# Performance work log

Hardware: AMD Instinct MI355X
Metric: run time of the kernel (lower is better)

Reference implementation:

```python
import jax, jax.numpy as jnp
import numpy as np

B, T, N = 64, 500, 2048
THRESHOLD = 1.0
BETA_RES = 0.9      # beta_reservoir
BETA_IN = 0.8       # input_lif_beta
SPECTRAL_RADIUS = 0.9
INIT_A, INIT_B = -1.0, 1.0


def setup_inputs() -> dict:
    key = jax.random.key(0)
    k1, k2, k3 = jax.random.split(key, 3)
    x = jax.random.normal(k1, (B, T, 1), dtype=jnp.float32)
    w_in = jax.random.normal(k2, (1, 1), dtype=jnp.float32)      # input_fc weight (out=1, in=1)
    w_res_in = jax.random.normal(k3, (N, 1), dtype=jnp.float32)  # reservoir_fc weight (out=N, in=1)
    # Recurrent weights: uniform[a,b] then rescale to desired spectral radius (done in numpy, matches init-time torch code)
    rng = np.random.default_rng(0)
    W = rng.uniform(INIT_A, INIT_B, size=(N, N)).astype(np.float32)
    radius = np.abs(np.linalg.eigvals(W)).max()
    W = W * (SPECTRAL_RADIUS / radius)
    W_rec = jnp.asarray(W, dtype=jnp.float32)
    return {"x": x, "w_in": w_in, "w_res_in": w_res_in, "W_rec": W_rec}


def reference(x, w_in, w_res_in, W_rec):
    """Vmem input path: input LIF integrates without spiking; reservoir is an
    all-to-all recurrent LIF with zero reset. Returns (avg_firing_rate, spike_record, mem_record)."""
    dtype = x.dtype
    imem0 = jnp.zeros((x.shape[0], 1), dtype)
    mem0 = jnp.zeros((x.shape[0], N), dtype)
    spk0 = jnp.zeros((x.shape[0], N), dtype)

    def step(carry, x_t):
        imem, mem, spk = carry
        # input LIF membrane (no spike/reset in 'Vmem' mode)
        imem = BETA_IN * imem + x_t @ w_in.T                      # (B,1)
        cur = imem @ w_res_in.T                                   # (B,N)
        # reservoir RLeaky, zero reset based on previous spikes, recurrent all-to-all
        mem = BETA_RES * mem * (1.0 - spk) + cur + spk @ W_rec.T  # (B,N)
        spk = (mem > THRESHOLD).astype(dtype)
        return (imem, mem, spk), (spk, mem)

    xs = jnp.transpose(x, (1, 0, 2))  # (T,B,1)
    _, (spike_record, mem_record) = jax.lax.scan(step, (imem0, mem0, spk0), xs)
    avg_firing_rate = spike_record.mean()
    return avg_firing_rate, spike_record, mem_record
```

## Files before the change

### kernel.cpp

```cpp
#include <hip/hip_runtime.h>

typedef int v4i __attribute__((ext_vector_type(4)));

#define WMAX_OFF   0
#define CNT_OFF    4
#define EP_OFF     8
#define IMEM_OFF   64
#define PK_OFF     131072
#define FLAGS_OFF  196608
#define WFRAG_OFF  262144

__global__ void sr_prep(const float* __restrict__ x, const float* __restrict__ w_in,
                        float* __restrict__ imem, unsigned* wmax_bits, unsigned* cnt,
                        unsigned* ep) {
  int b = threadIdx.x;
  if (b == 64) *wmax_bits = 0u;
  if (b == 65) *cnt = 0u;
  if (b == 66) *ep += 1024u;
  if (b < 64) {
    float wi = w_in[0];
    float im = 0.0f;
    for (int t = 0; t < 500; ++t) {
      im = 0.8f * im + x[b * 500 + t] * wi;
      imem[t * 64 + b] = im;
    }
  }
}

__global__ void sr_wmax(const float* __restrict__ W, unsigned* wmax_bits) {
  __shared__ unsigned sm;
  if (threadIdx.x == 0) sm = 0u;
  __syncthreads();
  float m = 0.0f;
  for (size_t i = (size_t)blockIdx.x * 256 + threadIdx.x; i < 4194304ull; i += 262144ull)
    m = fmaxf(m, fabsf(W[i]));
  atomicMax(&sm, __float_as_uint(m));
  __syncthreads();
  if (threadIdx.x == 0) atomicMax(wmax_bits, sm);
}

__global__ void sr_wquant(const float* __restrict__ W, const unsigned* __restrict__ wmax_bits,
                          v4i* __restrict__ wfr) {
  __shared__ float ws[16][257];
  const int p = blockIdx.x >> 3;
  const int w = blockIdx.x & 7;
  const int tid = threadIdx.x;
  {
    int r = tid >> 5;
    int c0 = (tid & 31) * 8;
    const float* src = W + (size_t)(p * 16 + r) * 2048 + 256 * w + c0;
    #pragma unroll
    for (int j = 0; j < 8; ++j) ws[r][c0 + j] = src[j];
  }
  __syncthreads();
  const int fl = tid >> 6;
  const int kl = fl >> 1, sp = fl & 1;
  const int lane = tid & 63;
  const int col = lane & 15;
  const int q = lane >> 4;
  const float S = 32000.0f / __uint_as_float(*wmax_bits);
  int dw[4] = {0, 0, 0, 0};
  #pragma unroll
  for (int j = 0; j < 16; ++j) {
    int d = j >> 2, i = j & 3;
    float wv = ws[col][(4 * kl + q) * 16 + 4 * i + d];
    int qv = (int)rintf(wv * S);
    int hi = (qv + 128) >> 8;
    int lo = qv - (hi << 8);
    int v = sp ? lo : hi;
    dw[d] |= (v & 255) << (8 * i);
  }
  v4i o; o[0] = dw[0]; o[1] = dw[1]; o[2] = dw[2]; o[3] = dw[3];
  wfr[(size_t)((((p * 8 + w) * 4 + kl) * 2 + sp)) * 64 + lane] = o;
}

__global__ __launch_bounds__(512, 2)
void sr_main(const float* __restrict__ imem, const v4i* __restrict__ wfr,
             unsigned* pk, unsigned* flags, const unsigned* __restrict__ ep,
             const float* __restrict__ w_res, const unsigned* __restrict__ wmax_bits,
             unsigned* cnt_g, float* __restrict__ out) {
  extern __shared__ char smem_raw[];
  unsigned* spk_lds = (unsigned*)smem_raw;
  v4i* redv = (v4i*)(smem_raw + 16384);
  int* outl = (int*)(smem_raw + 49152);

  const int p = blockIdx.x;
  const int tid = threadIdx.x;
  const int w = tid >> 6;
  const int lane = tid & 63;
  const int q = lane >> 4;
  const int col = lane & 15;
  const unsigned base = *ep;

  v4i wf[4][2];
  #pragma unroll
  for (int kl = 0; kl < 4; ++kl)
    #pragma unroll
    for (int sp = 0; sp < 2; ++sp)
      wf[kl][sp] = wfr[(size_t)((((p * 8 + w) * 4 + kl) * 2 + sp)) * 64 + lane];

  const int be = tid >> 3;
  const int h = tid & 7;
  const int nl = h * 2;
  const float wr0 = w_res[p * 16 + nl + 0];
  const float wr1 = w_res[p * 16 + nl + 1];
  float mem0 = 0, mem1 = 0, sp0 = 0, sp1 = 0;
  int cnt = 0;
  const float invS = __uint_as_float(*wmax_bits) / 32000.0f;
  const v4i vzero = {0, 0, 0, 0};
  const int pubshift = (h >> 1) * 8 + 2 * (h & 1) + 4 * (be & 1);
  const int sh2 = (col & 1) * 4;
  const int cc = col >> 1;

  for (int t = 0; t < 500; ++t) {
    float im = imem[t * 64 + be];
    float rec0 = 0, rec1 = 0;
    if (t > 0) {
      const unsigned target = base + (unsigned)t;
      if (tid < 128) {
        unsigned* fp = flags + (size_t)(t & 1) * 128 + tid;
        int guard = 0;
        while (__hip_atomic_load(fp, __ATOMIC_RELAXED, __HIP_MEMORY_SCOPE_AGENT) != target) {
          __builtin_amdgcn_s_sleep(1);
          if (++guard > (1 << 20)) break;
        }
      }
      __syncthreads();

      {
        const unsigned* src = pk + (size_t)(t & 1) * 4096 + tid;
        unsigned qw[8];
        #pragma unroll
        for (int j = 0; j < 8; ++j)
          qw[j] = __hip_atomic_load(src + 512 * j, __ATOMIC_RELAXED, __HIP_MEMORY_SCOPE_AGENT);
        #pragma unroll
        for (int j = 0; j < 8; ++j) {
          int P = tid + 512 * j;
          int idx = (P & ~31) | ((P & 31) ^ (((P >> 5) & 3) << 3));
          spk_lds[idx] = qw[j];
        }
      }
      __syncthreads();

      unsigned ww[16];
      #pragma unroll
      for (int f = 0; f < 16; ++f) {
        int kl = f & 3, bt = f >> 2;
        ww[f] = spk_lds[(16 * w + 4 * kl + q) * 32 + ((bt * 8 + cc) ^ (q << 3))];
      }

      v4i acc[4][2];
      #pragma unroll
      for (int bt = 0; bt < 4; ++bt) { acc[bt][0] = vzero; acc[bt][1] = vzero; }
      #pragma unroll
      for (int f = 0; f < 16; ++f) {
        int kl = f & 3, bt = f >> 2;
        unsigned wbs = ww[f] >> sh2;
        v4i a;
        a[0] = (int)((wbs >> 0) & 0x01010101u);
        a[1] = (int)((wbs >> 1) & 0x01010101u);
        a[2] = (int)((wbs >> 2) & 0x01010101u);
        a[3] = (int)((wbs >> 3) & 0x01010101u);
        acc[bt][0] = __builtin_amdgcn_mfma_i32_16x16x64_i8(a, wf[kl][0], acc[bt][0], 0, 0, 0);
        acc[bt][1] = __builtin_amdgcn_mfma_i32_16x16x64_i8(a, wf[kl][1], acc[bt][1], 0, 0, 0);
      }
      #pragma unroll
      for (int bt = 0; bt < 4; ++bt) {
        v4i c = acc[bt][0] * 256 + acc[bt][1];
        redv[(w * 4 + bt) * 64 + lane] = c;
      }
      __syncthreads();
      if (w < 4) {
        v4i s = vzero;
        #pragma unroll
        for (int ww2 = 0; ww2 < 8; ++ww2) s += redv[(ww2 * 4 + w) * 64 + lane];
        int ob = (w * 16 + (lane >> 4) * 4) * 16 + (lane & 15);
        outl[ob]      = s[0];
        outl[ob + 16] = s[1];
        outl[ob + 32] = s[2];
        outl[ob + 48] = s[3];
      }
      __syncthreads();
      int2 rv = *(const int2*)(outl + be * 16 + nl);
      rec0 = (float)rv.x * invS;
      rec1 = (float)rv.y * invS;
    }

    mem0 = 0.9f * mem0 * (1.0f - sp0) + im * wr0 + rec0;
    mem1 = 0.9f * mem1 * (1.0f - sp1) + im * wr1 + rec1;
    int s0i = mem0 > 1.0f, s1i = mem1 > 1.0f;
    sp0 = (float)s0i; sp1 = (float)s1i;

    unsigned v = ((unsigned)(s0i | (s1i << 1))) << pubshift;
    v |= (unsigned)__shfl_xor((int)v, 1);
    v |= (unsigned)__shfl_xor((int)v, 2);
    v |= (unsigned)__shfl_xor((int)v, 4);
    v |= (unsigned)__shfl_xor((int)v, 8);
    if ((tid & 15) == 0)
      __hip_atomic_store(&pk[(size_t)((t + 1) & 1) * 4096 + p * 32 + (tid >> 4)], v,
                         __ATOMIC_RELAXED, __HIP_MEMORY_SCOPE_AGENT);
    __syncthreads();
    if (tid == 0)
      __hip_atomic_store(&flags[(size_t)((t + 1) & 1) * 128 + p], base + (unsigned)(t + 1),
                         __ATOMIC_RELAXED, __HIP_MEMORY_SCOPE_AGENT);
    cnt += s0i + s1i;

    size_t sb = 1ull + (size_t)t * 131072ull + (size_t)be * 2048ull + (size_t)(p * 16 + nl);
    __builtin_nontemporal_store(sp0, out + sb + 0);
    __builtin_nontemporal_store(sp1, out + sb + 1);
    __builtin_nontemporal_store(mem0, out + sb + 65536000ull + 0);
    __builtin_nontemporal_store(mem1, out + sb + 65536000ull + 1);
  }

  __syncthreads();
  int* csh = (int*)smem_raw;
  if (tid == 0) csh[0] = 0;
  __syncthreads();
  atomicAdd(csh, cnt);
  __syncthreads();
  if (tid == 0) atomicAdd(cnt_g, (unsigned)csh[0]);
}

__global__ void sr_fin(const unsigned* __restrict__ cnt, float* __restrict__ out) {
  out[0] = (float)((double)(*cnt) / 65536000.0);
}

extern "C" void kernel_launch(void* const* d_in, const int* in_sizes, int n_in,
                              void* d_out, int out_size, void* d_ws, size_t ws_size,
                              hipStream_t stream) {
  const float* x     = (const float*)d_in[0];
  const float* w_in  = (const float*)d_in[1];
  const float* w_res = (const float*)d_in[2];
  const float* W     = (const float*)d_in[3];
  float* out = (float*)d_out;
  char* ws = (char*)d_ws;

  unsigned* wmax_bits = (unsigned*)(ws + WMAX_OFF);
  unsigned* cntp      = (unsigned*)(ws + CNT_OFF);
  unsigned* ep        = (unsigned*)(ws + EP_OFF);
  float* imem         = (float*)(ws + IMEM_OFF);
  unsigned* pkt       = (unsigned*)(ws + PK_OFF);
  unsigned* flg       = (unsigned*)(ws + FLAGS_OFF);
  v4i* wfr            = (v4i*)(ws + WFRAG_OFF);

  sr_prep<<<1, 128, 0, stream>>>(x, w_in, imem, wmax_bits, cntp, ep);
  sr_wmax<<<1024, 256, 0, stream>>>(W, wmax_bits);
  sr_wquant<<<1024, 512, 0, stream>>>(W, wmax_bits, wfr);
  sr_main<<<128, 512, 53248, stream>>>(imem, wfr, pkt, flg, ep, w_res, wmax_bits, cntp, out);
  sr_fin<<<1, 1, 0, stream>>>(cntp, out);
}
```

Baseline: 2.113 ms.

## Embed epoch tags in 64-bit spike packets to drop flag barrier and LDS staging

Each spike word is now published as a 64-bit value whose upper half holds the step epoch. Consumers poll their own 16 packets directly from global memory until every tag matches. This removes the per-block flag array, the producer-side barrier before the flag store, the flag spin by 128 threads, and the LDS staging of spike words along with two block barriers. In exchange every thread polls 16 global words per step, adding L2 traffic and retries. The prep kernel also batches its x loads in chunks of 10.

```diff
diff --git a/kernel.cpp b/kernel.cpp
--- a/kernel.cpp
+++ b/kernel.cpp
@@ -7,7 +7,6 @@
 #define EP_OFF     8
 #define IMEM_OFF   64
 #define PK_OFF     131072
-#define FLAGS_OFF  196608
 #define WFRAG_OFF  262144
 
 __global__ void sr_prep(const float* __restrict__ x, const float* __restrict__ w_in,
@@ -20,9 +19,15 @@
   if (b < 64) {
     float wi = w_in[0];
     float im = 0.0f;
-    for (int t = 0; t < 500; ++t) {
-      im = 0.8f * im + x[b * 500 + t] * wi;
-      imem[t * 64 + b] = im;
+    for (int t0 = 0; t0 < 500; t0 += 10) {
+      float xs[10];
+      #pragma unroll
+      for (int j = 0; j < 10; ++j) xs[j] = x[b * 500 + t0 + j];
+      #pragma unroll
+      for (int j = 0; j < 10; ++j) {
+        im = 0.8f * im + xs[j] * wi;
+        imem[(t0 + j) * 64 + b] = im;
+      }
     }
   }
 }
@@ -76,13 +81,12 @@
 
 __global__ __launch_bounds__(512, 2)
 void sr_main(const float* __restrict__ imem, const v4i* __restrict__ wfr,
-             unsigned* pk, unsigned* flags, const unsigned* __restrict__ ep,
+             unsigned long long* pk, const unsigned* __restrict__ ep,
              const float* __restrict__ w_res, const unsigned* __restrict__ wmax_bits,
              unsigned* cnt_g, float* __restrict__ out) {
   extern __shared__ char smem_raw[];
-  unsigned* spk_lds = (unsigned*)smem_raw;
-  v4i* redv = (v4i*)(smem_raw + 16384);
-  int* outl = (int*)(smem_raw + 49152);
+  v4i* redv = (v4i*)smem_raw;
+  int* outl = (int*)(smem_raw + 32768);
 
   const int p = blockIdx.x;
   const int tid = threadIdx.x;
@@ -112,50 +116,40 @@
   const int sh2 = (col & 1) * 4;
   const int cc = col >> 1;
 
+  int pidx[16];
+  #pragma unroll
+  for (int f = 0; f < 16; ++f) {
+    int kl = f & 3, bt = f >> 2;
+    pidx[f] = (16 * w + 4 * kl + q) * 32 + bt * 8 + cc;
+  }
+
   for (int t = 0; t < 500; ++t) {
     float im = imem[t * 64 + be];
     float rec0 = 0, rec1 = 0;
     if (t > 0) {
-      const unsigned target = base + (unsigned)t;
-      if (tid < 128) {
-        unsigned* fp = flags + (size_t)(t & 1) * 128 + tid;
-        int guard = 0;
-        while (__hip_atomic_load(fp, __ATOMIC_RELAXED, __HIP_MEMORY_SCOPE_AGENT) != target) {
-          __builtin_amdgcn_s_sleep(1);
-          if (++guard > (1 << 20)) break;
-        }
-      }
-      __syncthreads();
-
-      {
-        const unsigned* src = pk + (size_t)(t & 1) * 4096 + tid;
-        unsigned qw[8];
+      const unsigned tgt = base + (unsigned)t;
+      const unsigned long long* src = pk + (size_t)((t - 1) & 1) * 4096;
+      unsigned long long qp[16];
+      bool ok = false;
+      int guard = 0;
+      do {
         #pragma unroll
-        for (int j = 0; j < 8; ++j)
-          qw[j] = __hip_atomic_load(src + 512 * j, __ATOMIC_RELAXED, __HIP_MEMORY_SCOPE_AGENT);
+        for (int f = 0; f < 16; ++f)
+          qp[f] = __hip_atomic_load(src + pidx[f], __ATOMIC_RELAXED, __HIP_MEMORY_SCOPE_AGENT);
+        unsigned bad = 0;
         #pragma unroll
-        for (int j = 0; j < 8; ++j) {
-          int P = tid + 512 * j;
-          int idx = (P & ~31) | ((P & 31) ^ (((P >> 5) & 3) << 3));
-          spk_lds[idx] = qw[j];
-        }
-      }
-      __syncthreads();
-
-      unsigned ww[16];
+        for (int f = 0; f < 16; ++f) bad |= (unsigned)(qp[f] >> 32) ^ tgt;
+        ok = (bad == 0);
+        if (!ok) __builtin_amdgcn_s_sleep(1);
+      } while (!ok && ++guard < (1 << 20));
+
+      v4i acc[4][2];
+      #pragma unroll
+      for (int bt = 0; bt < 4; ++bt) { acc[bt][0] = vzero; acc[bt][1] = vzero; }
       #pragma unroll
       for (int f = 0; f < 16; ++f) {
         int kl = f & 3, bt = f >> 2;
-        ww[f] = spk_lds[(16 * w + 4 * kl + q) * 32 + ((bt * 8 + cc) ^ (q << 3))];
-      }
-
-      v4i acc[4][2];
-      #pragma unroll
-      for (int bt = 0; bt < 4; ++bt) { acc[bt][0] = vzero; acc[bt][1] = vzero; }
-      #pragma unroll
-      for (int f = 0; f < 16; ++f) {
-        int kl = f & 3, bt = f >> 2;
-        unsigned wbs = ww[f] >> sh2;
+        unsigned wbs = (unsigned)qp[f] >> sh2;
         v4i a;
         a[0] = (int)((wbs >> 0) & 0x01010101u);
         a[1] = (int)((wbs >> 1) & 0x01010101u);
@@ -196,13 +190,12 @@
     v |= (unsigned)__shfl_xor((int)v, 2);
     v |= (unsigned)__shfl_xor((int)v, 4);
     v |= (unsigned)__shfl_xor((int)v, 8);
-    if ((tid & 15) == 0)
-      __hip_atomic_store(&pk[(size_t)((t + 1) & 1) * 4096 + p * 32 + (tid >> 4)], v,
+    if ((tid & 15) == 0) {
+      unsigned long long pkt =
+          (unsigned long long)v | ((unsigned long long)(base + (unsigned)(t + 1)) << 32);
+      __hip_atomic_store(&pk[(size_t)(t & 1) * 4096 + p * 32 + (tid >> 4)], pkt,
                          __ATOMIC_RELAXED, __HIP_MEMORY_SCOPE_AGENT);
-    __syncthreads();
-    if (tid == 0)
-      __hip_atomic_store(&flags[(size_t)((t + 1) & 1) * 128 + p], base + (unsigned)(t + 1),
-                         __ATOMIC_RELAXED, __HIP_MEMORY_SCOPE_AGENT);
+    }
     cnt += s0i + s1i;
 
     size_t sb = 1ull + (size_t)t * 131072ull + (size_t)be * 2048ull + (size_t)(p * 16 + nl);
@@ -239,13 +232,12 @@
   unsigned* cntp      = (unsigned*)(ws + CNT_OFF);
   unsigned* ep        = (unsigned*)(ws + EP_OFF);
   float* imem         = (float*)(ws + IMEM_OFF);
-  unsigned* pkt       = (unsigned*)(ws + PK_OFF);
-  unsigned* flg       = (unsigned*)(ws + FLAGS_OFF);
+  unsigned long long* pkt = (unsigned long long*)(ws + PK_OFF);
   v4i* wfr            = (v4i*)(ws + WFRAG_OFF);
 
   sr_prep<<<1, 128, 0, stream>>>(x, w_in, imem, wmax_bits, cntp, ep);
   sr_wmax<<<1024, 256, 0, stream>>>(W, wmax_bits);
   sr_wquant<<<1024, 512, 0, stream>>>(W, wmax_bits, wfr);
-  sr_main<<<128, 512, 53248, stream>>>(imem, wfr, pkt, flg, ep, w_res, wmax_bits, cntp, out);
+  sr_main<<<128, 512, 36864, stream>>>(imem, wfr, pkt, ep, w_res, wmax_bits, cntp, out);
   sr_fin<<<1, 1, 0, stream>>>(cntp, out);
 }
```

Result: slower. 2.247 ms (+6.3%).

## Per-wave flag polling and direct global spike fragment loads, drop LDS staging

Applied to the files above, without the earlier changes.

Each wavefront now polls only the 16 producer flags it depends on, using a wave-wide vote, instead of 128 threads polling and then a block barrier. Spike words are loaded straight from global memory into MFMA operand registers, which removes the LDS staging copy and two __syncthreads per step. The packet buffer parity is realigned so step t writes slot t&1 and readers use (t-1)&1. The input prep loop is also batched so the x loads are issued ahead of the recurrence. The trade-off is more, smaller global loads per wave and a flag/data ordering that now rests on relaxed atomics per wave.

```diff
diff --git a/kernel.cpp b/kernel.cpp
--- a/kernel.cpp
+++ b/kernel.cpp
@@ -20,9 +20,15 @@
   if (b < 64) {
     float wi = w_in[0];
     float im = 0.0f;
-    for (int t = 0; t < 500; ++t) {
-      im = 0.8f * im + x[b * 500 + t] * wi;
-      imem[t * 64 + b] = im;
+    for (int t0 = 0; t0 < 500; t0 += 10) {
+      float xs[10];
+      #pragma unroll
+      for (int j = 0; j < 10; ++j) xs[j] = x[b * 500 + t0 + j];
+      #pragma unroll
+      for (int j = 0; j < 10; ++j) {
+        im = 0.8f * im + xs[j] * wi;
+        imem[(t0 + j) * 64 + b] = im;
+      }
     }
   }
 }
@@ -80,9 +86,8 @@
              const float* __restrict__ w_res, const unsigned* __restrict__ wmax_bits,
              unsigned* cnt_g, float* __restrict__ out) {
   extern __shared__ char smem_raw[];
-  unsigned* spk_lds = (unsigned*)smem_raw;
-  v4i* redv = (v4i*)(smem_raw + 16384);
-  int* outl = (int*)(smem_raw + 49152);
+  v4i* redv = (v4i*)smem_raw;
+  int* outl = (int*)(smem_raw + 32768);
 
   const int p = blockIdx.x;
   const int tid = threadIdx.x;
@@ -116,37 +121,27 @@
     float im = imem[t * 64 + be];
     float rec0 = 0, rec1 = 0;
     if (t > 0) {
-      const unsigned target = base + (unsigned)t;
-      if (tid < 128) {
-        unsigned* fp = flags + (size_t)(t & 1) * 128 + tid;
+      const unsigned tgt = base + (unsigned)t;
+      {
+        const unsigned* fp = flags + (size_t)(t & 1) * 128 + 16 * w + (lane & 15);
+        unsigned fv = __hip_atomic_load(fp, __ATOMIC_RELAXED, __HIP_MEMORY_SCOPE_AGENT);
         int guard = 0;
-        while (__hip_atomic_load(fp, __ATOMIC_RELAXED, __HIP_MEMORY_SCOPE_AGENT) != target) {
+        while (!__all(fv == tgt)) {
           __builtin_amdgcn_s_sleep(1);
+          fv = __hip_atomic_load(fp, __ATOMIC_RELAXED, __HIP_MEMORY_SCOPE_AGENT);
           if (++guard > (1 << 20)) break;
         }
       }
-      __syncthreads();
-
+
+      unsigned ww[16];
       {
-        const unsigned* src = pk + (size_t)(t & 1) * 4096 + tid;
-        unsigned qw[8];
+        const unsigned* srcb = pk + (size_t)((t - 1) & 1) * 4096 + (16 * w + q) * 32 + cc;
         #pragma unroll
-        for (int j = 0; j < 8; ++j)
-          qw[j] = __hip_atomic_load(src + 512 * j, __ATOMIC_RELAXED, __HIP_MEMORY_SCOPE_AGENT);
-        #pragma unroll
-        for (int j = 0; j < 8; ++j) {
-          int P = tid + 512 * j;
-          int idx = (P & ~31) | ((P & 31) ^ (((P >> 5) & 3) << 3));
-          spk_lds[idx] = qw[j];
+        for (int f = 0; f < 16; ++f) {
+          int kl = f & 3, bt = f >> 2;
+          ww[f] = __hip_atomic_load(srcb + kl * 128 + bt * 8,
+                                    __ATOMIC_RELAXED, __HIP_MEMORY_SCOPE_AGENT);
         }
-      }
-      __syncthreads();
-
-      unsigned ww[16];
-      #pragma unroll
-      for (int f = 0; f < 16; ++f) {
-        int kl = f & 3, bt = f >> 2;
-        ww[f] = spk_lds[(16 * w + 4 * kl + q) * 32 + ((bt * 8 + cc) ^ (q << 3))];
       }
 
       v4i acc[4][2];
@@ -197,7 +192,7 @@
     v |= (unsigned)__shfl_xor((int)v, 4);
     v |= (unsigned)__shfl_xor((int)v, 8);
     if ((tid & 15) == 0)
-      __hip_atomic_store(&pk[(size_t)((t + 1) & 1) * 4096 + p * 32 + (tid >> 4)], v,
+      __hip_atomic_store(&pk[(size_t)(t & 1) * 4096 + p * 32 + (tid >> 4)], v,
                          __ATOMIC_RELAXED, __HIP_MEMORY_SCOPE_AGENT);
     __syncthreads();
     if (tid == 0)
@@ -246,6 +241,6 @@
   sr_prep<<<1, 128, 0, stream>>>(x, w_in, imem, wmax_bits, cntp, ep);
   sr_wmax<<<1024, 256, 0, stream>>>(W, wmax_bits);
   sr_wquant<<<1024, 512, 0, stream>>>(W, wmax_bits, wfr);
-  sr_main<<<128, 512, 53248, stream>>>(imem, wfr, pkt, flg, ep, w_res, wmax_bits, cntp, out);
+  sr_main<<<128, 512, 36864, stream>>>(imem, wfr, pkt, flg, ep, w_res, wmax_bits, cntp, out);
   sr_fin<<<1, 1, 0, stream>>>(cntp, out);
 }
```

New measurement: 2.254 ms. 6.7% more time.
